# Kernel tuning notes

Measured on AMD Instinct MI355X. Metric: run time of the kernel, lower is better.

Reference implementation:

```python
import jax, jax.numpy as jnp
import numpy as np

GROUPS = 2
STRIDE = (1, 1)
PADDING = ((1, 1), (1, 1))
DILATION = (1, 1)


def setup_inputs() -> dict:
    key = jax.random.key(0)
    k1, k2, k3 = jax.random.split(key, 3)
    B, Cin, H, W = 16, 256, 112, 112
    Cout, kH, kW = 256, 3, 3
    x = jax.random.normal(k1, (B, Cin, H, W), dtype=jnp.float32)
    # kaiming_uniform-like scale: fan_in = (Cin/groups)*kH*kW
    fan_in = (Cin // GROUPS) * kH * kW
    bound = float(np.sqrt(1.0 / fan_in))
    weight = jax.random.uniform(k2, (Cout, Cin // GROUPS, kH, kW), dtype=jnp.float32,
                                minval=-bound, maxval=bound)
    bias = jax.random.uniform(k3, (Cout,), dtype=jnp.float32, minval=-bound, maxval=bound)
    return {"x": x, "weight": weight, "bias": bias}


def reference(x, weight, bias):
    # Grouped conv2d: every backend path of SparseGroupedConv2d (sparse triton
    # active-tile kernel, zero-tile skip, dense F.conv2d fallback) computes this
    # exact grouped convolution; the tile machinery only skips zero-energy tiles.
    y = jax.lax.conv_general_dilated(
        x, weight,
        window_strides=STRIDE,
        padding=PADDING,
        rhs_dilation=DILATION,
        dimension_numbers=("NCHW", "OIHW", "NCHW"),
        feature_group_count=GROUPS,
    )
    return y + bias[None, :, None, None]
```

## Files before the change

### kernel.cpp

```cpp
#include <hip/hip_runtime.h>
#include <hip/hip_bf16.h>
#include <stdint.h>

#define BATCH 16
#define CIN   256
#define HH    112
#define WW    112
#define GROUPS 2
#define CG    128
#define COG   128
#define RH    4
#define CK    32
#define NCHUNK (CG/CK)

typedef __bf16 bf16x8 __attribute__((ext_vector_type(8)));
typedef float  f32x4  __attribute__((ext_vector_type(4)));

#define WB_BYTES   (GROUPS*3*3*COG*CG*2)
#define ZBUF_OFF   WB_BYTES
#define ZBUF_BYTES 8192
#define XB_OFF     (ZBUF_OFF + ZBUF_BYTES)
#define XB_BYTES   ((size_t)BATCH*HH*WW*CIN*2)
#define WS_NEED    ((size_t)XB_OFF + XB_BYTES)

__device__ inline void load_lds16(const void* g, void* l) {
    __builtin_amdgcn_global_load_lds(
        (const __attribute__((address_space(1))) void*)g,
        (__attribute__((address_space(3))) void*)l, 16, 0, 0);
}

__global__ __launch_bounds__(256) void k_wcvt(const float* __restrict__ w,
                                              ushort* __restrict__ wb) {
    int i = blockIdx.x * 256 + threadIdx.x;
    int ci = i & 127;
    int t  = i >> 7;
    int co = t & 127;
    t >>= 7;
    int kw = t % 3; t /= 3;
    int kh = t % 3;
    int g  = t / 3;
    int src = (((g*COG + co)*CG + ci)*3 + kh)*3 + kw;
    __hip_bfloat16 v = __float2bfloat16(w[src]);
    wb[i] = *reinterpret_cast<ushort*>(&v);
}

#define XPAD 113
__global__ __launch_bounds__(256) void k_xcvt(const float* __restrict__ x,
                                              ushort* __restrict__ xb) {
    __shared__ float tile[64 * XPAD];
    int bid = blockIdx.x;
    int cc  = bid & 3;
    int h   = (bid >> 2) % HH;
    int b   = bid / (4 * HH);
    int tid = threadIdx.x;

    const float* src = x + ((size_t)(b*CIN + cc*64) * HH + h) * WW;
    for (int tt = tid; tt < 64*28; tt += 256) {
        int c = tt / 28, v = tt % 28;
        float4 f = *reinterpret_cast<const float4*>(src + (size_t)c*HH*WW + v*4);
        float* d = &tile[c*XPAD + v*4];
        d[0]=f.x; d[1]=f.y; d[2]=f.z; d[3]=f.w;
    }
    __syncthreads();

    if (tid < 224) {
        int w = tid >> 1, half = tid & 1;
        ushort o[32];
#pragma unroll
        for (int j = 0; j < 32; ++j) {
            __hip_bfloat16 v = __float2bfloat16(tile[(half*32 + j)*XPAD + w]);
            o[j] = *reinterpret_cast<ushort*>(&v);
        }
        ushort* dst = xb + (((size_t)(b*HH + h)*WW + w)*CIN + cc*64 + half*32);
        const uint4* o4 = reinterpret_cast<const uint4*>(o);
        uint4* d4 = reinterpret_cast<uint4*>(dst);
        d4[0]=o4[0]; d4[1]=o4[1]; d4[2]=o4[2]; d4[3]=o4[3];
    }
}

__device__ inline void stage_w(const ushort* __restrict__ wb, ushort* dstbuf,
                               int g, int kkw, int chunk, int wave, int lane) {
    int co = wave*16 + (lane >> 2);
    int t  = (lane & 3) ^ ((lane >> 3) & 3);
    const ushort* src = wb + (((size_t)(g*9 + kkw)*COG + co)*CG + chunk*CK + t*8);
    load_lds16(src, dstbuf + wave*16*CK);
}

__global__ __launch_bounds__(512, 2) void k_conv(const ushort* __restrict__ xb,
                                                 const ushort* __restrict__ wb,
                                                 const float* __restrict__ bias,
                                                 float* __restrict__ out,
                                                 const ushort* __restrict__ zbuf) {
    __shared__ __align__(16) ushort xs[6*114*CK];
    __shared__ __align__(16) ushort wsb[2][COG*CK];

    int bid = blockIdx.x;
    int g   = bid / 448;
    int r   = bid % 448;
    int b   = r / 28;
    int q   = r % 28;
    int oh0 = q * RH;

    int tid  = threadIdx.x;
    int wave = tid >> 6;
    int lane = tid & 63;
    int wm   = wave >> 2;
    int wr   = wave & 3;
    int l15  = lane & 15;
    int lk   = lane >> 4;

    if (tid < 384) {
        int rr = tid / 64, wcol = (tid >> 5) & 1, c = tid & 31;
        xs[(rr*114 + wcol*113)*CK + c] = 0;
    }

    int sA = lk ^ ((l15 >> 1) & 3);
    int qv = lane >> 2;

    f32x4 acc[4][7];
#pragma unroll
    for (int m = 0; m < 4; ++m)
#pragma unroll
        for (int n = 0; n < 7; ++n) acc[m][n] = f32x4{0.f,0.f,0.f,0.f};

    for (int chunk = 0; chunk < NCHUNK; ++chunk) {
        for (int t = wave; t < 42; t += 8) {
            int rr = t / 7, ii = t % 7;
            int h    = oh0 - 1 + rr;
            int w_in = ii*16 + qv;
            int ts   = (lane & 3) ^ (((2*rr + 1 + qv) >> 1) & 3);
            const ushort* src;
            if (h >= 0 && h < HH)
                src = xb + (((size_t)(b*HH + h)*WW + w_in)*CIN + g*CG + chunk*CK + ts*8);
            else
                src = zbuf + lane*8;
            load_lds16(src, &xs[(rr*114 + 1 + ii*16)*CK]);
        }
        stage_w(wb, wsb[0], g, 0, chunk, wave, lane);
        __syncthreads();

        for (int kkw = 0; kkw < 9; ++kkw) {
            int cur = kkw & 1;
            if (kkw < 8) stage_w(wb, wsb[cur ^ 1], g, kkw + 1, chunk, wave, lane);
            int kh = kkw / 3, kw = kkw - kh*3;

            int sB = lk ^ (((2*(wr + kh) + l15 + kw) >> 1) & 3);
            const ushort* bbase = &xs[((wr + kh)*114 + l15 + kw)*CK + sB*8];
            bf16x8 bfr[7];
#pragma unroll
            for (int n = 0; n < 7; ++n)
                bfr[n] = *reinterpret_cast<const bf16x8*>(bbase + n*16*CK);

            const ushort* wrow = wsb[cur];
            const ushort* abase = &wrow[(wm*64 + l15)*CK + sA*8];
#pragma unroll
            for (int m = 0; m < 4; ++m) {
                bf16x8 afr = *reinterpret_cast<const bf16x8*>(abase + m*16*CK);
#pragma unroll
                for (int n = 0; n < 7; ++n)
                    acc[m][n] = __builtin_amdgcn_mfma_f32_16x16x32_bf16(
                        afr, bfr[n], acc[m][n], 0, 0, 0);
            }
            __syncthreads();
        }
    }

    int oh = oh0 + wr;
#pragma unroll
    for (int m = 0; m < 4; ++m) {
        int cob = g*CG + wm*64 + m*16 + lk*4;
#pragma unroll
        for (int j = 0; j < 4; ++j) {
            int co = cob + j;
            float bv = bias[co];
            float* orow = out + (((size_t)(b*CIN + co)*HH + oh)*WW);
#pragma unroll
            for (int n = 0; n < 7; ++n)
                orow[n*16 + l15] = acc[m][n][j] + bv;
        }
    }
}

__global__ __launch_bounds__(128) void k_direct(const float* __restrict__ x,
                                                const float* __restrict__ w,
                                                const float* __restrict__ bias,
                                                float* __restrict__ out) {
    int bid = blockIdx.x;
    int oh  = bid % HH;
    int t   = bid / HH;
    int co  = t % CIN;
    int b   = t / CIN;
    int ow  = threadIdx.x;
    if (ow >= WW) return;
    int g = co / COG;
    float s = bias[co];
    const float* wp = w + (size_t)co*CG*9;
    const float* xp = x + ((size_t)b*CIN + g*CG)*HH*WW;
    for (int ci = 0; ci < CG; ++ci) {
        const float* xr = xp + (size_t)ci*HH*WW;
        const float* wr_ = wp + ci*9;
#pragma unroll
        for (int kh = 0; kh < 3; ++kh) {
            int ih = oh + kh - 1;
            if (ih < 0 || ih >= HH) continue;
#pragma unroll
            for (int kw = 0; kw < 3; ++kw) {
                int iw = ow + kw - 1;
                if (iw < 0 || iw >= WW) continue;
                s += xr[ih*WW + iw] * wr_[kh*3 + kw];
            }
        }
    }
    out[(((size_t)b*CIN + co)*HH + oh)*WW + ow] = s;
}

extern "C" void kernel_launch(void* const* d_in, const int* in_sizes, int n_in,
                              void* d_out, int out_size, void* d_ws, size_t ws_size,
                              hipStream_t stream) {
    const float* x    = (const float*)d_in[0];
    const float* w    = (const float*)d_in[1];
    const float* bias = (const float*)d_in[2];
    float* out        = (float*)d_out;

    if (ws_size >= WS_NEED) {
        ushort* wb   = (ushort*)d_ws;
        ushort* zb   = (ushort*)((char*)d_ws + ZBUF_OFF);
        ushort* xbuf = (ushort*)((char*)d_ws + XB_OFF);
        hipMemsetAsync(zb, 0, ZBUF_BYTES, stream);
        k_wcvt<<<1152, 256, 0, stream>>>(w, wb);
        k_xcvt<<<BATCH*HH*4, 256, 0, stream>>>(x, xbuf);
        k_conv<<<896, 512, 0, stream>>>(xbuf, wb, bias, out, zb);
    } else {
        k_direct<<<BATCH*CIN*HH, 128, 0, stream>>>(x, w, bias, out);
    }
}
```

Before: 236.7 us.

## Double-buffer input chunks and stage all nine weight taps per chunk

Restructures the conv main loop so each channel chunk stages all nine weight taps into LDS at once. The next chunk's input tile is prefetched into a second LDS buffer while the current chunk computes. This cuts block-wide barriers from one per tap to about two per chunk and overlaps input loads with MFMA work. In exchange LDS use rises to roughly 158 KB per block, which likely allows only one 512-thread block per CU instead of two. Weight staging for the next chunk also now sits between barriers rather than overlapping compute.

New measurement: 225.1 us. -4.9%, faster.

```diff
diff --git a/kernel.cpp b/kernel.cpp
--- a/kernel.cpp
+++ b/kernel.cpp
@@ -78,12 +78,31 @@
     }
 }
 
-__device__ inline void stage_w(const ushort* __restrict__ wb, ushort* dstbuf,
-                               int g, int kkw, int chunk, int wave, int lane) {
+__device__ inline void stage_w_all(const ushort* __restrict__ wb, ushort* wsb,
+                                   int g, int chunk, int wave, int lane) {
     int co = wave*16 + (lane >> 2);
     int t  = (lane & 3) ^ ((lane >> 3) & 3);
-    const ushort* src = wb + (((size_t)(g*9 + kkw)*COG + co)*CG + chunk*CK + t*8);
-    load_lds16(src, dstbuf + wave*16*CK);
+#pragma unroll
+    for (int tap = 0; tap < 9; ++tap) {
+        const ushort* src = wb + (((size_t)(g*9 + tap)*COG + co)*CG + chunk*CK + t*8);
+        load_lds16(src, wsb + (tap*COG + wave*16)*CK);
+    }
+}
+
+__device__ inline void stage_x(const ushort* __restrict__ xb, ushort* dst,
+                               const ushort* __restrict__ zbuf,
+                               int b, int g, int oh0, int chunk, int wave, int lane) {
+    int qv = lane >> 2;
+    for (int t = wave; t < 42; t += 8) {
+        int rr = t / 7, ii = t % 7;
+        int h    = oh0 - 1 + rr;
+        int w_in = ii*16 + qv;
+        int ts   = (lane & 3) ^ (((2*rr + 1 + qv) >> 1) & 3);
+        const ushort* src = (h >= 0 && h < HH)
+            ? xb + (((size_t)(b*HH + h)*WW + w_in)*CIN + g*CG + chunk*CK + ts*8)
+            : zbuf + lane*8;
+        load_lds16(src, dst + (rr*114 + 1 + ii*16)*CK);
+    }
 }
 
 __global__ __launch_bounds__(512, 2) void k_conv(const ushort* __restrict__ xb,
@@ -91,8 +110,8 @@
                                                  const float* __restrict__ bias,
                                                  float* __restrict__ out,
                                                  const ushort* __restrict__ zbuf) {
-    __shared__ __align__(16) ushort xs[6*114*CK];
-    __shared__ __align__(16) ushort wsb[2][COG*CK];
+    __shared__ __align__(16) ushort xs[2][6*114*CK];
+    __shared__ __align__(16) ushort wsb[9*COG*CK];
 
     int bid = blockIdx.x;
     int g   = bid / 448;
@@ -109,13 +128,13 @@
     int l15  = lane & 15;
     int lk   = lane >> 4;
 
-    if (tid < 384) {
-        int rr = tid / 64, wcol = (tid >> 5) & 1, c = tid & 31;
-        xs[(rr*114 + wcol*113)*CK + c] = 0;
+    for (int t = tid; t < 768; t += 512) {
+        int buf = t / 384, r2 = t % 384;
+        int rr = r2 / 64, wcol = (r2 >> 5) & 1, c = r2 & 31;
+        xs[buf][(rr*114 + wcol*113)*CK + c] = 0;
     }
 
     int sA = lk ^ ((l15 >> 1) & 3);
-    int qv = lane >> 2;
 
     f32x4 acc[4][7];
 #pragma unroll
@@ -123,36 +142,27 @@
 #pragma unroll
         for (int n = 0; n < 7; ++n) acc[m][n] = f32x4{0.f,0.f,0.f,0.f};
 
-    for (int chunk = 0; chunk < NCHUNK; ++chunk) {
-        for (int t = wave; t < 42; t += 8) {
-            int rr = t / 7, ii = t % 7;
-            int h    = oh0 - 1 + rr;
-            int w_in = ii*16 + qv;
-            int ts   = (lane & 3) ^ (((2*rr + 1 + qv) >> 1) & 3);
-            const ushort* src;
-            if (h >= 0 && h < HH)
-                src = xb + (((size_t)(b*HH + h)*WW + w_in)*CIN + g*CG + chunk*CK + ts*8);
-            else
-                src = zbuf + lane*8;
-            load_lds16(src, &xs[(rr*114 + 1 + ii*16)*CK]);
-        }
-        stage_w(wb, wsb[0], g, 0, chunk, wave, lane);
-        __syncthreads();
-
+    stage_x(xb, xs[0], zbuf, b, g, oh0, 0, wave, lane);
+    stage_w_all(wb, wsb, g, 0, wave, lane);
+    __syncthreads();
+
+#pragma unroll 1
+    for (int c = 0; c < NCHUNK; ++c) {
+        const ushort* xcur = xs[c & 1];
+        if (c + 1 < NCHUNK)
+            stage_x(xb, xs[(c + 1) & 1], zbuf, b, g, oh0, c + 1, wave, lane);
+
+#pragma unroll
         for (int kkw = 0; kkw < 9; ++kkw) {
-            int cur = kkw & 1;
-            if (kkw < 8) stage_w(wb, wsb[cur ^ 1], g, kkw + 1, chunk, wave, lane);
-            int kh = kkw / 3, kw = kkw - kh*3;
-
+            const int kh = kkw / 3, kw = kkw - kh*3;
             int sB = lk ^ (((2*(wr + kh) + l15 + kw) >> 1) & 3);
-            const ushort* bbase = &xs[((wr + kh)*114 + l15 + kw)*CK + sB*8];
+            const ushort* bbase = &xcur[((wr + kh)*114 + l15 + kw)*CK + sB*8];
             bf16x8 bfr[7];
 #pragma unroll
             for (int n = 0; n < 7; ++n)
                 bfr[n] = *reinterpret_cast<const bf16x8*>(bbase + n*16*CK);
 
-            const ushort* wrow = wsb[cur];
-            const ushort* abase = &wrow[(wm*64 + l15)*CK + sA*8];
+            const ushort* abase = &wsb[(kkw*COG + wm*64 + l15)*CK + sA*8];
 #pragma unroll
             for (int m = 0; m < 4; ++m) {
                 bf16x8 afr = *reinterpret_cast<const bf16x8*>(abase + m*16*CK);
@@ -161,8 +171,16 @@
                     acc[m][n] = __builtin_amdgcn_mfma_f32_16x16x32_bf16(
                         afr, bfr[n], acc[m][n], 0, 0, 0);
             }
-            __syncthreads();
-        }
+        }
+
+        __builtin_amdgcn_sched_barrier(0);
+        asm volatile("s_waitcnt lgkmcnt(0)" ::: "memory");
+        __builtin_amdgcn_s_barrier();
+
+        if (c + 1 < NCHUNK)
+            stage_w_all(wb, wsb, g, c + 1, wave, lane);
+
+        __syncthreads();
     }
 
     int oh = oh0 + wr;
```
